# Kernel optimization log

Hardware: AMD Instinct MI355X
Metric: run time of the kernel (lower is better)

The kernel has to match this reference:

```python
import jax, jax.numpy as jnp
import numpy as np

B, S, H, E, V = 256, 512, 512, 128, 30000
RNN_IN = H + E + 1  # weighted context + id embedding + rate


def setup_inputs() -> dict:
    key = jax.random.key(0)
    ks = jax.random.split(key, 16)
    nrm = lambda k, shape, s=0.02: jax.random.normal(k, shape, dtype=jnp.float32) * s
    return {
        "input_id": jax.random.randint(ks[0], (B, 1), 0, V),
        "input_rate": jax.random.uniform(ks[1], (B, 1), dtype=jnp.float32),
        "hidden": nrm(ks[2], (1, B, H), 1.0),
        "encoder_outputs": nrm(ks[3], (S, B, H), 1.0),
        "attn_mask": jax.random.randint(ks[4], (B, S), 0, 2),
        "constraint_vec": (jax.random.uniform(ks[5], (B, V)) > 0.3).astype(jnp.float32),
        "emb_id": nrm(ks[6], (V, E)),
        "attn_w": nrm(ks[7], (2 * H, H)),
        "attn_b": jnp.zeros((H,), jnp.float32),
        "v_w": nrm(ks[8], (H,)),
        "w_ih": nrm(ks[9], (3 * H, RNN_IN)),
        "w_hh": nrm(ks[10], (3 * H, H)),
        "b_ih": jnp.zeros((3 * H,), jnp.float32),
        "b_hh": jnp.zeros((3 * H,), jnp.float32),
        "fc_id_w": nrm(ks[11], (H, V)),
        "fc_id_b": jnp.zeros((V,), jnp.float32),
        "tandem_w": nrm(ks[12], (E + H, H)),
        "tandem_b": jnp.zeros((H,), jnp.float32),
        "rate_w": nrm(ks[13], (H, 1)),
        "rate_b": jnp.zeros((1,), jnp.float32),
    }


def reference(input_id, input_rate, hidden, encoder_outputs, attn_mask,
              constraint_vec, emb_id, attn_w, attn_b, v_w,
              w_ih, w_hh, b_ih, b_hh, fc_id_w, fc_id_b,
              tandem_w, tandem_b, rate_w, rate_b):
    hd = hidden.shape[-1]
    h0 = hidden[0]                                # [B, H]
    embedded = emb_id[input_id[:, 0]]             # [B, E] (dropout p=0 -> identity)

    # --- additive attention (concat-linear split to avoid [B,S,2H] concat) ---
    enc = jnp.transpose(encoder_outputs, (1, 0, 2))         # [B, S, H]
    hid_part = h0 @ attn_w[:hd]                             # [B, H]
    enc_part = jnp.einsum('bsh,hk->bsk', enc, attn_w[hd:])  # [B, S, H]
    energy = jnp.tanh(hid_part[:, None, :] + enc_part + attn_b)
    scores = jnp.einsum('bsh,h->bs', energy, v_w)           # [B, S]
    scores = jnp.where(attn_mask == 0, jnp.float32(-1e10), scores)
    a = jax.nn.softmax(scores, axis=1)
    weighted = jnp.einsum('bs,bsh->bh', a, enc)             # [B, H]

    # --- GRU cell (torch gate order: r, z, n) ---
    x = jnp.concatenate([weighted, embedded, input_rate], axis=1)  # [B, H+E+1]
    gi = x @ w_ih.T + b_ih
    gh = h0 @ w_hh.T + b_hh
    gi_r, gi_z, gi_n = jnp.split(gi, 3, axis=1)
    gh_r, gh_z, gh_n = jnp.split(gh, 3, axis=1)
    r = jax.nn.sigmoid(gi_r + gh_r)
    z = jax.nn.sigmoid(gi_z + gh_z)
    n = jnp.tanh(gi_n + r * gh_n)
    h1 = (1.0 - z) * n + z * h0                   # [B, H]

    # --- masked log-softmax over id vocabulary ---
    logits = h1 @ fc_id_w + fc_id_b               # [B, V]
    maxes = jnp.max(logits, axis=1, keepdims=True)
    x_exp = jnp.exp(logits - maxes) * constraint_vec
    pred = jnp.clip(x_exp / jnp.sum(x_exp, axis=1, keepdims=True), 1e-6, 1.0)
    prediction_id = jnp.log(pred)

    # --- tandem rate head ---
    max_id = jnp.argmax(prediction_id, axis=1)
    id_emb = emb_id[max_id]                       # [B, E]
    rate_in = jax.nn.relu(jnp.concatenate([id_emb, h1], axis=1) @ tandem_w + tandem_b)
    prediction_rate = jax.nn.sigmoid(rate_in @ rate_w + rate_b)  # [B, 1]

    return prediction_id, prediction_rate, h1[None]  # hidden [1, B, H]
```

## Files before the change

### kernel.cpp

```cpp
#include <hip/hip_runtime.h>
#include <hip/hip_bf16.h>

#define B_ 256
#define S_ 512
#define H_ 512
#define E_ 128
#define V_ 30000
#define RNNIN_ 641

using bf16x8 = __attribute__((ext_vector_type(8))) short;
using f32x4  = __attribute__((ext_vector_type(4))) float;

__device__ __forceinline__ short f2bf(float f) {
  unsigned int u = __float_as_uint(f);
  u += 0x7fffu + ((u >> 16) & 1u);
  return (short)(u >> 16);
}

__device__ __forceinline__ float fast_tanh(float x) {
  x = fminf(10.f, fmaxf(-10.f, x));
  float t = __expf(2.f * x);
  return (t - 1.f) / (t + 1.f);
}

__device__ __forceinline__ float sigmoidf(float x) {
  return 1.f / (1.f + __expf(-x));
}

__device__ void gemm_nn_dev(float (*As)[65], float (*Bs)[65],
    const float* __restrict__ A, const float* __restrict__ Bm,
    const float* __restrict__ bias, float* __restrict__ C,
    int M, int N, int K, int m0, int n0)
{
  const int tid = threadIdx.x;
  const int tx = tid & 15, ty = tid >> 4;
  float acc[4][4] = {};
  for (int k0 = 0; k0 < K; k0 += 16) {
    __syncthreads();
    #pragma unroll
    for (int i = 0; i < 4; i++) {
      int e = tid + i * 256;
      int m = e >> 4, k = e & 15;
      float v = 0.f;
      if (m0 + m < M && k0 + k < K) v = A[(size_t)(m0 + m) * K + k0 + k];
      As[k][m] = v;
    }
    #pragma unroll
    for (int i = 0; i < 4; i++) {
      int e = tid + i * 256;
      int k = e >> 6, n = e & 63;
      float v = 0.f;
      if (n0 + n < N && k0 + k < K) v = Bm[(size_t)(k0 + k) * N + n0 + n];
      Bs[k][n] = v;
    }
    __syncthreads();
    #pragma unroll
    for (int k = 0; k < 16; k++) {
      float a[4], b[4];
      #pragma unroll
      for (int i = 0; i < 4; i++) a[i] = As[k][ty * 4 + i];
      #pragma unroll
      for (int j = 0; j < 4; j++) b[j] = Bs[k][tx * 4 + j];
      #pragma unroll
      for (int i = 0; i < 4; i++)
        #pragma unroll
        for (int j = 0; j < 4; j++) acc[i][j] += a[i] * b[j];
    }
  }
  #pragma unroll
  for (int i = 0; i < 4; i++) {
    int m = m0 + ty * 4 + i;
    if (m >= M) continue;
    #pragma unroll
    for (int j = 0; j < 4; j++) {
      int n = n0 + tx * 4 + j;
      if (n >= N) continue;
      C[(size_t)m * N + n] = acc[i][j] + bias[n];
    }
  }
}

__device__ void gemm_bt_dev(float (*As)[65], float (*Bs)[65],
    const float* __restrict__ A, const float* __restrict__ Bm,
    const float* __restrict__ bias, float* __restrict__ C,
    int M, int N, int K)
{
  const int m0 = blockIdx.x * 64, n0 = blockIdx.y * 64;
  const int tid = threadIdx.x;
  const int tx = tid & 15, ty = tid >> 4;
  float acc[4][4] = {};
  for (int k0 = 0; k0 < K; k0 += 16) {
    __syncthreads();
    #pragma unroll
    for (int i = 0; i < 4; i++) {
      int e = tid + i * 256;
      int m = e >> 4, k = e & 15;
      float v = 0.f;
      if (m0 + m < M && k0 + k < K) v = A[(size_t)(m0 + m) * K + k0 + k];
      As[k][m] = v;
    }
    #pragma unroll
    for (int i = 0; i < 4; i++) {
      int e = tid + i * 256;
      int n = e >> 4, k = e & 15;
      float v = 0.f;
      if (n0 + n < N && k0 + k < K) v = Bm[(size_t)(n0 + n) * K + k0 + k];
      Bs[k][n] = v;
    }
    __syncthreads();
    #pragma unroll
    for (int k = 0; k < 16; k++) {
      float a[4], b[4];
      #pragma unroll
      for (int i = 0; i < 4; i++) a[i] = As[k][ty * 4 + i];
      #pragma unroll
      for (int j = 0; j < 4; j++) b[j] = Bs[k][tx * 4 + j];
      #pragma unroll
      for (int i = 0; i < 4; i++)
        #pragma unroll
        for (int j = 0; j < 4; j++) acc[i][j] += a[i] * b[j];
    }
  }
  #pragma unroll
  for (int i = 0; i < 4; i++) {
    int m = m0 + ty * 4 + i;
    if (m >= M) continue;
    #pragma unroll
    for (int j = 0; j < 4; j++) {
      int n = n0 + tx * 4 + j;
      if (n >= N) continue;
      C[(size_t)m * N + n] = acc[i][j] + bias[n];
    }
  }
}

__global__ __launch_bounds__(256) void prep_fused(
    const float* __restrict__ attn_w, unsigned short* __restrict__ Btf,
    const float* __restrict__ hidden, const float* __restrict__ attn_b,
    float* __restrict__ hid_pb)
{
  __shared__ float As[16][65];
  __shared__ float Bs[16][65];
  int bid = blockIdx.x;
  if (bid < 1024) {
    int i = bid * 256 + threadIdx.x;
    int k = i >> 9, n = i & 511;
    float v = attn_w[(size_t)H_ * H_ + i];
    int idx = ((((k >> 5) * 32 + (n >> 4)) * 4 + ((k >> 3) & 3)) * 16 + (n & 15)) * 8 + (k & 7);
    Btf[idx] = (unsigned short)f2bf(v);
  } else {
    int bb = bid - 1024;
    gemm_nn_dev(As, Bs, hidden, attn_w, attn_b, hid_pb, B_, H_, H_,
                (bb & 3) * 64, (bb >> 2) * 64);
  }
}

__global__ __launch_bounds__(256) void attn_gemm_score(
    const float* __restrict__ A, const unsigned short* __restrict__ Btf,
    const float* __restrict__ hid_pb, const float* __restrict__ v_w,
    float* __restrict__ scores)
{
  __shared__ short As[2 * 4096];

  const int bid  = blockIdx.x;
  const int tile = (bid & 7) * 512 + (bid >> 3);
  const int mblk = tile >> 1, nblk = tile & 1;
  const int m0 = mblk * 64, n0 = nblk * 256;

  const int tid  = threadIdx.x;
  const int lane = tid & 63;
  const int wv   = tid >> 6;
  const int quad = lane >> 4, l15 = lane & 15;

  const int arow = tid >> 2, aseg = tid & 3;
  const float* aptr = A + (size_t)(m0 + arow) * H_ + aseg * 16;
  const int ac = aseg >> 1, aq0 = (aseg & 1) * 2;
  short* aw0 = &As[((ac * 4 + (arow >> 4)) * 64 + aq0 * 16 + (arow & 15)) * 8];

  const int nf0 = nblk * 16 + wv * 4;

  f32x4 acc[4][4];
  #pragma unroll
  for (int i = 0; i < 4; i++)
    #pragma unroll
    for (int j = 0; j < 4; j++) acc[i][j] = f32x4{0.f, 0.f, 0.f, 0.f};

  float4 rA[4];
  #pragma unroll
  for (int i = 0; i < 4; i++) rA[i] = *(const float4*)(aptr + i * 4);

  #pragma unroll
  for (int kt = 0; kt < 8; kt++) {
    bf16x8 b[2][4];
    #pragma unroll
    for (int kc = 0; kc < 2; kc++)
      #pragma unroll
      for (int tj = 0; tj < 4; tj++)
        b[kc][tj] = *(const bf16x8*)(Btf + (((kt * 2 + kc) * 32 + nf0 + tj) << 9) + lane * 8);

    {
      bf16x8 f0, f1;
      f0[0] = f2bf(rA[0].x); f0[1] = f2bf(rA[0].y); f0[2] = f2bf(rA[0].z); f0[3] = f2bf(rA[0].w);
      f0[4] = f2bf(rA[1].x); f0[5] = f2bf(rA[1].y); f0[6] = f2bf(rA[1].z); f0[7] = f2bf(rA[1].w);
      f1[0] = f2bf(rA[2].x); f1[1] = f2bf(rA[2].y); f1[2] = f2bf(rA[2].z); f1[3] = f2bf(rA[2].w);
      f1[4] = f2bf(rA[3].x); f1[5] = f2bf(rA[3].y); f1[6] = f2bf(rA[3].z); f1[7] = f2bf(rA[3].w);
      *(bf16x8*)(aw0 + (kt & 1) * 4096)       = f0;
      *(bf16x8*)(aw0 + (kt & 1) * 4096 + 128) = f1;
    }

    if (kt < 7) {
      const float* an = aptr + (kt + 1) * 64;
      #pragma unroll
      for (int i = 0; i < 4; i++) rA[i] = *(const float4*)(an + i * 4);
    }

    asm volatile("s_waitcnt lgkmcnt(0)" ::: "memory");
    __builtin_amdgcn_s_barrier();
    __builtin_amdgcn_sched_barrier(0);

    const short* ab = &As[(kt & 1) * 4096];
    #pragma unroll
    for (int kc = 0; kc < 2; kc++) {
      bf16x8 a[4];
      #pragma unroll
      for (int mi = 0; mi < 4; mi++)
        a[mi] = *(const bf16x8*)&ab[((kc * 4 + mi) * 64 + lane) * 8];
      #pragma unroll
      for (int mi = 0; mi < 4; mi++)
        #pragma unroll
        for (int tj = 0; tj < 4; tj++)
          acc[mi][tj] = __builtin_amdgcn_mfma_f32_16x16x32_bf16(a[mi], b[kc][tj], acc[mi][tj], 0, 0, 0);
    }
  }

  __syncthreads();
  float* part = (float*)As;
  #pragma unroll
  for (int ti = 0; ti < 4; ti++) {
    #pragma unroll
    for (int r = 0; r < 4; r++) {
      int m = m0 + ti * 16 + quad * 4 + r;
      int b = m & (B_ - 1);
      float sum = 0.f;
      #pragma unroll
      for (int tj = 0; tj < 4; tj++) {
        int n = n0 + wv * 64 + tj * 16 + l15;
        float v = acc[ti][tj][r] + hid_pb[b * H_ + n];
        sum += fast_tanh(v) * v_w[n];
      }
      sum += __shfl_xor(sum, 1);
      sum += __shfl_xor(sum, 2);
      sum += __shfl_xor(sum, 4);
      sum += __shfl_xor(sum, 8);
      if (l15 == 0) part[(ti * 16 + quad * 4 + r) * 4 + wv] = sum;
    }
  }
  __syncthreads();
  if (tid < 64) {
    float s4 = part[tid * 4 + 0] + part[tid * 4 + 1] + part[tid * 4 + 2] + part[tid * 4 + 3];
    int m = m0 + tid;
    atomicAdd(scores + (m & (B_ - 1)) * S_ + (m >> 8), s4);
  }
}

__global__ __launch_bounds__(256) void gemm_gru(
    const float* __restrict__ xb, const float* __restrict__ w_ih,
    const float* __restrict__ b_ih, float* __restrict__ gi,
    const float* __restrict__ hid, const float* __restrict__ w_hh,
    const float* __restrict__ b_hh, float* __restrict__ gh)
{
  __shared__ float As[16][65];
  __shared__ float Bs[16][65];
  if (blockIdx.z == 0) gemm_bt_dev(As, Bs, xb, w_ih, b_ih, gi, B_, 1536, RNNIN_);
  else                 gemm_bt_dev(As, Bs, hid, w_hh, b_hh, gh, B_, 1536, H_);
}

__global__ __launch_bounds__(256, 4) void logits_gemm(
    const unsigned short* __restrict__ Ab, const float* __restrict__ Bw,
    const float* __restrict__ bias, float* __restrict__ C)
{
  __shared__ short As[2 * 16 * 64 * 8];
  __shared__ short Bs[2 * 4 * 64 * 8];
  const int n0 = blockIdx.x * 64;
  const int tid = threadIdx.x;
  const int lane = tid & 63;
  const int wv = tid >> 6;
  const int quad = lane >> 4, l15 = lane & 15;

  f32x4 acc[4][4];
  #pragma unroll
  for (int i = 0; i < 4; i++)
    #pragma unroll
    for (int j = 0; j < 4; j++) acc[i][j] = f32x4{0.f, 0.f, 0.f, 0.f};

  const int nB  = tid & 63;
  const int kg  = tid >> 6;
  const int cB  = kg >> 1;
  const int q0  = (kg & 1) * 2;
  const int tjB = nB >> 4;
  const bool nOK = (n0 + nB) < V_;

  for (int kt = 0; kt < 8; kt++) {
    const int kb = kt * 64;
    __syncthreads();
    #pragma unroll
    for (int p = 0; p < 8; p++) {
      int m = p * 32 + (tid >> 3), f = tid & 7;
      int c = f >> 2, q = f & 3;
      bf16x8 v = *(const bf16x8*)(Ab + (size_t)m * H_ + kb + c * 32 + q * 8);
      int mt = m >> 4, ld = q * 16 + (m & 15);
      *(bf16x8*)&As[((c * 16 + mt) * 64 + ld) * 8] = v;
    }
    {
      float col[16];
      const float* src = Bw + (size_t)(kb + kg * 16) * V_ + n0 + nB;
      #pragma unroll
      for (int i = 0; i < 16; i++) col[i] = nOK ? src[(size_t)i * V_] : 0.f;
      bf16x8 f0, f1;
      #pragma unroll
      for (int i = 0; i < 8; i++) { f0[i] = f2bf(col[i]); f1[i] = f2bf(col[8 + i]); }
      int ld0 = q0 * 16 + (nB & 15);
      *(bf16x8*)&Bs[((cB * 4 + tjB) * 64 + ld0) * 8] = f0;
      *(bf16x8*)&Bs[((cB * 4 + tjB) * 64 + ld0 + 16) * 8] = f1;
    }
    __syncthreads();
    #pragma unroll
    for (int c = 0; c < 2; c++) {
      bf16x8 a[4], b[4];
      #pragma unroll
      for (int ti = 0; ti < 4; ti++)
        a[ti] = *(const bf16x8*)&As[((c * 16 + wv * 4 + ti) * 64 + lane) * 8];
      #pragma unroll
      for (int tj = 0; tj < 4; tj++)
        b[tj] = *(const bf16x8*)&Bs[((c * 4 + tj) * 64 + lane) * 8];
      #pragma unroll
      for (int ti = 0; ti < 4; ti++)
        #pragma unroll
        for (int tj = 0; tj < 4; tj++)
          acc[ti][tj] = __builtin_amdgcn_mfma_f32_16x16x32_bf16(a[ti], b[tj], acc[ti][tj], 0, 0, 0);
    }
  }
  #pragma unroll
  for (int ti = 0; ti < 4; ti++)
    #pragma unroll
    for (int r = 0; r < 4; r++) {
      int m = wv * 64 + ti * 16 + quad * 4 + r;
      #pragma unroll
      for (int tj = 0; tj < 4; tj++) {
        int n = n0 + tj * 16 + l15;
        if (n < V_) C[(size_t)m * V_ + n] = acc[ti][tj][r] + bias[n];
      }
    }
}

__global__ __launch_bounds__(256) void attn_softmax(
    const float* __restrict__ scores, const int* __restrict__ mask, float* __restrict__ aw)
{
  int b = blockIdx.x, tid = threadIdx.x;
  __shared__ float red[256];
  float v0 = scores[b * S_ + tid];
  float v1 = scores[b * S_ + tid + 256];
  if (mask[b * S_ + tid] == 0) v0 = -1e10f;
  if (mask[b * S_ + tid + 256] == 0) v1 = -1e10f;
  red[tid] = fmaxf(v0, v1);
  __syncthreads();
  for (int off = 128; off; off >>= 1) { if (tid < off) red[tid] = fmaxf(red[tid], red[tid + off]); __syncthreads(); }
  float mx = red[0];
  __syncthreads();
  float e0 = __expf(v0 - mx), e1 = __expf(v1 - mx);
  red[tid] = e0 + e1;
  __syncthreads();
  for (int off = 128; off; off >>= 1) { if (tid < off) red[tid] += red[tid + off]; __syncthreads(); }
  float inv = 1.f / red[0];
  aw[b * S_ + tid] = e0 * inv;
  aw[b * S_ + tid + 256] = e1 * inv;
}

__global__ __launch_bounds__(512) void attn_weighted_part(
    const float* __restrict__ aw, const float* __restrict__ enc, float* __restrict__ wpart)
{
  int b = blockIdx.x, c = blockIdx.y, h = threadIdx.x;
  __shared__ float a_s[64];
  if (h < 64) a_s[h] = aw[b * S_ + c * 64 + h];
  __syncthreads();
  const float* ep = enc + ((size_t)(c * 64) * B_ + b) * H_ + h;
  float acc = 0.f;
  #pragma unroll 8
  for (int s = 0; s < 64; s++)
    acc += a_s[s] * ep[(size_t)s * B_ * H_];
  wpart[((size_t)c * B_ + b) * H_ + h] = acc;
}

__global__ void build_x(const float* __restrict__ wpart, const int* __restrict__ ids,
                        const float* __restrict__ emb, const float* __restrict__ rate,
                        float* __restrict__ x)
{
  int i = blockIdx.x * 256 + threadIdx.x;
  if (i >= B_ * RNNIN_) return;
  int b = i / RNNIN_, j = i % RNNIN_;
  float v;
  if (j < H_) {
    size_t o = (size_t)b * H_ + j;
    const size_t st = (size_t)B_ * H_;
    v = 0.f;
    #pragma unroll
    for (int c = 0; c < 8; c++) v += wpart[o + c * st];
  }
  else if (j < H_ + E_) v = emb[(size_t)ids[b] * E_ + (j - H_)];
  else v = rate[b];
  x[i] = v;
}

__global__ void gru_gates(const float* __restrict__ gi, const float* __restrict__ gh,
                          const float* __restrict__ h0, float* __restrict__ h1,
                          unsigned short* __restrict__ h1b, float* __restrict__ h1_out)
{
  int i = blockIdx.x * 256 + threadIdx.x;
  int b = i >> 9, j = i & (H_ - 1);
  const float* gib = gi + (size_t)b * 1536;
  const float* ghb = gh + (size_t)b * 1536;
  float r = sigmoidf(gib[j] + ghb[j]);
  float z = sigmoidf(gib[512 + j] + ghb[512 + j]);
  float n = fast_tanh(gib[1024 + j] + r * ghb[1024 + j]);
  float h = (1.f - z) * n + z * h0[i];
  h1[i] = h;
  h1b[i] = (unsigned short)f2bf(h);
  h1_out[i] = h;
}

__global__ __launch_bounds__(1024) void softmax_fused(
    float* __restrict__ lp, const float* __restrict__ cv, int* __restrict__ maxid)
{
  int b = blockIdx.x, tid = threadIdx.x;
  int wid = tid >> 6, lane = tid & 63;
  float* row = lp + (size_t)b * V_;
  const float* cvr = cv + (size_t)b * V_;
  __shared__ float redf[16];
  __shared__ float rede[16];
  __shared__ int   redi[16];

  float mx = -INFINITY;
  for (int v = tid; v < V_; v += 1024) mx = fmaxf(mx, row[v]);
  #pragma unroll
  for (int o = 1; o < 64; o <<= 1) mx = fmaxf(mx, __shfl_xor(mx, o));
  if (lane == 0) redf[wid] = mx;
  __syncthreads();
  if (tid == 0) {
    float m = redf[0];
    for (int i = 1; i < 16; i++) m = fmaxf(m, redf[i]);
    redf[0] = m;
  }
  __syncthreads();
  float M = redf[0];
  __syncthreads();

  float s = 0.f, best = -1.f;
  int bi = 0;
  for (int v = tid; v < V_; v += 1024) {
    float e = __expf(row[v] - M) * cvr[v];
    row[v] = e;
    s += e;
    if (e > best) { best = e; bi = v; }
  }
  #pragma unroll
  for (int o = 1; o < 64; o <<= 1) {
    s += __shfl_xor(s, o);
    float ob = __shfl_xor(best, o);
    int oi = __shfl_xor(bi, o);
    if (ob > best || (ob == best && oi < bi)) { best = ob; bi = oi; }
  }
  if (lane == 0) { redf[wid] = s; rede[wid] = best; redi[wid] = bi; }
  __syncthreads();
  if (tid == 0) {
    float ss = 0.f, bb = rede[0];
    int ii = redi[0];
    for (int i = 0; i < 16; i++) {
      ss += redf[i];
      if (rede[i] > bb || (rede[i] == bb && redi[i] < ii)) { bb = rede[i]; ii = redi[i]; }
    }
    redf[0] = ss;
    maxid[b] = ii;
  }
  __syncthreads();
  float inv = 1.f / redf[0];
  for (int v = tid; v < V_; v += 1024) {
    float p = row[v] * inv;
    p = fminf(fmaxf(p, 1e-6f), 1.f);
    row[v] = __logf(p);
  }
}

__global__ __launch_bounds__(256) void tandem_gemm(
    const int* __restrict__ maxid, const float* __restrict__ emb,
    const float* __restrict__ h1, const float* __restrict__ tan_w,
    const float* __restrict__ tan_b, float* __restrict__ rate_in)
{
  __shared__ float As[16][65];
  __shared__ float Bs[16][65];
  const int m0 = blockIdx.x * 64, n0 = blockIdx.y * 64;
  const int tid = threadIdx.x;
  const int tx = tid & 15, ty = tid >> 4;
  float acc[4][4] = {};
  for (int k0 = 0; k0 < 640; k0 += 16) {
    __syncthreads();
    #pragma unroll
    for (int i = 0; i < 4; i++) {
      int e = tid + i * 256;
      int m = e >> 4, kk = e & 15;
      int mm = m0 + m, k = k0 + kk;
      float v = (k < E_) ? emb[(size_t)maxid[mm] * E_ + k]
                         : h1[(size_t)mm * H_ + (k - E_)];
      As[kk][m] = v;
    }
    #pragma unroll
    for (int i = 0; i < 4; i++) {
      int e = tid + i * 256;
      int k = e >> 6, n = e & 63;
      Bs[k][n] = tan_w[(size_t)(k0 + k) * H_ + n0 + n];
    }
    __syncthreads();
    #pragma unroll
    for (int k = 0; k < 16; k++) {
      float a[4], b[4];
      #pragma unroll
      for (int i = 0; i < 4; i++) a[i] = As[k][ty * 4 + i];
      #pragma unroll
      for (int j = 0; j < 4; j++) b[j] = Bs[k][tx * 4 + j];
      #pragma unroll
      for (int i = 0; i < 4; i++)
        #pragma unroll
        for (int j = 0; j < 4; j++) acc[i][j] += a[i] * b[j];
    }
  }
  #pragma unroll
  for (int i = 0; i < 4; i++) {
    int m = m0 + ty * 4 + i;
    #pragma unroll
    for (int j = 0; j < 4; j++) {
      int n = n0 + tx * 4 + j;
      rate_in[(size_t)m * H_ + n] = fmaxf(acc[i][j] + tan_b[n], 0.f);
    }
  }
}

__global__ __launch_bounds__(64) void rate_head(const float* __restrict__ rate_in,
                                                const float* __restrict__ rate_w,
                                                const float* __restrict__ rate_b,
                                                float* __restrict__ out)
{
  int b = blockIdx.x, t = threadIdx.x;
  float s = 0.f;
  #pragma unroll
  for (int i = 0; i < 8; i++) s += rate_in[b * H_ + t + 64 * i] * rate_w[t + 64 * i];
  #pragma unroll
  for (int m = 32; m; m >>= 1) s += __shfl_xor(s, m);
  if (t == 0) out[b] = sigmoidf(s + rate_b[0]);
}

extern "C" void kernel_launch(void* const* d_in, const int* in_sizes, int n_in,
                              void* d_out, int out_size, void* d_ws, size_t ws_size,
                              hipStream_t stream)
{
  const int*   input_id   = (const int*)  d_in[0];
  const float* input_rate = (const float*)d_in[1];
  const float* hidden     = (const float*)d_in[2];
  const float* enc        = (const float*)d_in[3];
  const int*   attn_mask  = (const int*)  d_in[4];
  const float* cv         = (const float*)d_in[5];
  const float* emb        = (const float*)d_in[6];
  const float* attn_w     = (const float*)d_in[7];
  const float* attn_b     = (const float*)d_in[8];
  const float* v_w        = (const float*)d_in[9];
  const float* w_ih       = (const float*)d_in[10];
  const float* w_hh       = (const float*)d_in[11];
  const float* b_ih       = (const float*)d_in[12];
  const float* b_hh       = (const float*)d_in[13];
  const float* fc_w       = (const float*)d_in[14];
  const float* fc_b       = (const float*)d_in[15];
  const float* tan_w      = (const float*)d_in[16];
  const float* tan_b      = (const float*)d_in[17];
  const float* rate_w     = (const float*)d_in[18];
  const float* rate_b     = (const float*)d_in[19];

  float* out = (float*)d_out;
  float* ws  = (float*)d_ws;
  float* hid_pb   = ws;
  float* scores   = ws + 131072;
  float* aw       = ws + 262144;
  float* xbuf     = ws + 524288;
  float* gi       = ws + 688384;
  float* gh       = ws + 1081600;
  float* h1       = ws + 1474816;
  float* rate_in  = ws + 1605888;
  int*   maxid    = (int*)(ws + 1736960);
  unsigned short* Btf = (unsigned short*)(ws + 1737216);
  unsigned short* h1b = (unsigned short*)(ws + 1868288);
  float* wpart = gi;

  float* out_pred = out;
  float* out_rate = out + (size_t)B_ * V_;
  float* out_h1   = out + (size_t)B_ * V_ + B_;

  hipMemsetAsync(scores, 0, (size_t)B_ * S_ * sizeof(float), stream);

  prep_fused<<<1056, 256, 0, stream>>>(attn_w, Btf, hidden, attn_b, hid_pb);

  attn_gemm_score<<<4096, 256, 0, stream>>>(enc, Btf, hid_pb, v_w, scores);

  attn_softmax<<<B_, 256, 0, stream>>>(scores, attn_mask, aw);
  attn_weighted_part<<<dim3(B_, 8), 512, 0, stream>>>(aw, enc, wpart);
  build_x<<<641, 256, 0, stream>>>(wpart, input_id, emb, input_rate, xbuf);

  gemm_gru<<<dim3(4, 24, 2), 256, 0, stream>>>(xbuf, w_ih, b_ih, gi, hidden, w_hh, b_hh, gh);
  gru_gates<<<512, 256, 0, stream>>>(gi, gh, hidden, h1, h1b, out_h1);

  logits_gemm<<<469, 256, 0, stream>>>(h1b, fc_w, fc_b, out_pred);
  softmax_fused<<<B_, 1024, 0, stream>>>(out_pred, cv, maxid);

  tandem_gemm<<<dim3(4, 8), 256, 0, stream>>>(maxid, emb, h1, tan_w, tan_b, rate_in);
  rate_head<<<B_, 64, 0, stream>>>(rate_in, rate_w, rate_b, out_rate);
}
```

Measured before the change: 1.004 ms.

## Restructure attention score GEMM as persistent 512-thread blocks with LDS-resident weights

The attention score kernel now uses 1024 blocks of 512 threads. Each block loads a 128-column quarter of the bf16 attention weight matrix once into 128KB of LDS via global_load_lds and then loops over four 128-row tiles of encoder outputs. This removes the repeated per-tile global reads of B fragments. The encoder rows are prefetched in registers across k-steps and across tiles. In exchange, the large LDS footprint limits occupancy to one block per CU, and the per-k-step barriers with a small MFMA count per step may expose latency.

Measured after the change: 1.084 ms. 7.9% more time.

```diff
diff --git a/kernel.cpp b/kernel.cpp
--- a/kernel.cpp
+++ b/kernel.cpp
@@ -25,6 +25,12 @@
 
 __device__ __forceinline__ float sigmoidf(float x) {
   return 1.f / (1.f + __expf(-x));
+}
+
+__device__ __forceinline__ void gload_lds16(const void* g, void* l) {
+  __builtin_amdgcn_global_load_lds(
+      (const __attribute__((address_space(1))) void*)g,
+      (__attribute__((address_space(3))) void*)l, 16, 0, 0);
 }
 
 __device__ void gemm_nn_dev(float (*As)[65], float (*Bs)[65],
@@ -155,112 +161,149 @@
   }
 }
 
-__global__ __launch_bounds__(256) void attn_gemm_score(
+__global__ __launch_bounds__(512) void attn_gemm_score(
     const float* __restrict__ A, const unsigned short* __restrict__ Btf,
     const float* __restrict__ hid_pb, const float* __restrict__ v_w,
     float* __restrict__ scores)
 {
-  __shared__ short As[2 * 4096];
-
-  const int bid  = blockIdx.x;
-  const int tile = (bid & 7) * 512 + (bid >> 3);
-  const int mblk = tile >> 1, nblk = tile & 1;
-  const int m0 = mblk * 64, n0 = nblk * 256;
+  __shared__ short Bs[65536];
+  __shared__ short Abuf[8192];
+
+  const int bid = blockIdx.x;
+  const int w   = bid >> 8;
+  const int i8  = bid & 255;
+  const int q   = (i8 >> 3) & 3;
+  const int mg  = w * 64 + (i8 >> 5) * 8 + (i8 & 7);
+  const int nq0 = q * 128;
 
   const int tid  = threadIdx.x;
   const int lane = tid & 63;
   const int wv   = tid >> 6;
+  const int wr   = wv >> 2;
+  const int wc   = wv & 3;
   const int quad = lane >> 4, l15 = lane & 15;
 
-  const int arow = tid >> 2, aseg = tid & 3;
-  const float* aptr = A + (size_t)(m0 + arow) * H_ + aseg * 16;
-  const int ac = aseg >> 1, aq0 = (aseg & 1) * 2;
-  short* aw0 = &As[((ac * 4 + (arow >> 4)) * 64 + aq0 * 16 + (arow & 15)) * 8];
-
-  const int nf0 = nblk * 16 + wv * 4;
-
-  f32x4 acc[4][4];
-  #pragma unroll
-  for (int i = 0; i < 4; i++)
-    #pragma unroll
-    for (int j = 0; j < 4; j++) acc[i][j] = f32x4{0.f, 0.f, 0.f, 0.f};
-
-  float4 rA[4];
-  #pragma unroll
-  for (int i = 0; i < 4; i++) rA[i] = *(const float4*)(aptr + i * 4);
-
-  #pragma unroll
-  for (int kt = 0; kt < 8; kt++) {
-    bf16x8 b[2][4];
-    #pragma unroll
-    for (int kc = 0; kc < 2; kc++)
-      #pragma unroll
-      for (int tj = 0; tj < 4; tj++)
-        b[kc][tj] = *(const bf16x8*)(Btf + (((kt * 2 + kc) * 32 + nf0 + tj) << 9) + lane * 8);
-
-    {
-      bf16x8 f0, f1;
-      f0[0] = f2bf(rA[0].x); f0[1] = f2bf(rA[0].y); f0[2] = f2bf(rA[0].z); f0[3] = f2bf(rA[0].w);
-      f0[4] = f2bf(rA[1].x); f0[5] = f2bf(rA[1].y); f0[6] = f2bf(rA[1].z); f0[7] = f2bf(rA[1].w);
-      f1[0] = f2bf(rA[2].x); f1[1] = f2bf(rA[2].y); f1[2] = f2bf(rA[2].z); f1[3] = f2bf(rA[2].w);
-      f1[4] = f2bf(rA[3].x); f1[5] = f2bf(rA[3].y); f1[6] = f2bf(rA[3].z); f1[7] = f2bf(rA[3].w);
-      *(bf16x8*)(aw0 + (kt & 1) * 4096)       = f0;
-      *(bf16x8*)(aw0 + (kt & 1) * 4096 + 128) = f1;
-    }
-
-    if (kt < 7) {
-      const float* an = aptr + (kt + 1) * 64;
-      #pragma unroll
-      for (int i = 0; i < 4; i++) rA[i] = *(const float4*)(an + i * 4);
-    }
-
+  #pragma unroll
+  for (int i = 0; i < 16; i++) {
+    int frag = wv * 16 + i;
+    const unsigned short* g = Btf
+        + ((size_t)((frag >> 3) * 32 + q * 8 + (frag & 7)) << 9) + lane * 8;
+    gload_lds16((const void*)g, (void*)(Bs + (size_t)frag * 512));
+  }
+
+  const int rt = tid >> 2, qs = tid & 3;
+  const float* tb = A + ((size_t)mg * 512 + rt) * H_ + qs * 8;
+  short* awp = Abuf + (((rt >> 4) * 64) + qs * 16 + (rt & 15)) * 8;
+
+  const float vw0 = v_w[nq0 + wc * 32 + l15];
+  const float vw1 = v_w[nq0 + wc * 32 + 16 + l15];
+
+  float4 s0a = *(const float4*)(tb);
+  float4 s0b = *(const float4*)(tb + 4);
+  float4 s1a = *(const float4*)(tb + 32);
+  float4 s1b = *(const float4*)(tb + 36);
+  float4 s2a = *(const float4*)(tb + 64);
+  float4 s2b = *(const float4*)(tb + 68);
+  float4 s3a = *(const float4*)(tb + 96);
+  float4 s3b = *(const float4*)(tb + 100);
+
+  asm volatile("s_waitcnt vmcnt(0)" ::: "memory");
+  __builtin_amdgcn_s_barrier();
+
+  f32x4 acc[4][2];
+  #pragma unroll
+  for (int mi = 0; mi < 4; mi++) {
+    acc[mi][0] = f32x4{0.f, 0.f, 0.f, 0.f};
+    acc[mi][1] = f32x4{0.f, 0.f, 0.f, 0.f};
+  }
+
+#define KT_STEP(kt, SA, SB)                                                   \
+  do {                                                                        \
+    { bf16x8 f;                                                               \
+      f[0] = f2bf(SA.x); f[1] = f2bf(SA.y); f[2] = f2bf(SA.z); f[3] = f2bf(SA.w); \
+      f[4] = f2bf(SB.x); f[5] = f2bf(SB.y); f[6] = f2bf(SB.z); f[7] = f2bf(SB.w); \
+      *(bf16x8*)(awp + ((kt) & 1) * 4096) = f; }                              \
+    if ((kt) < 12) {                                                          \
+      SA = *(const float4*)(tba + ((kt) + 4) * 32);                           \
+      SB = *(const float4*)(tba + ((kt) + 4) * 32 + 4);                       \
+    } else if (t < 3) {                                                       \
+      SA = *(const float4*)(tba + 65536 + ((kt) - 12) * 32);                  \
+      SB = *(const float4*)(tba + 65536 + ((kt) - 12) * 32 + 4);              \
+    }                                                                         \
+    asm volatile("s_waitcnt lgkmcnt(0)" ::: "memory");                        \
+    __builtin_amdgcn_s_barrier();                                             \
+    __builtin_amdgcn_sched_barrier(0);                                        \
+    { const short* ap = Abuf + ((kt) & 1) * 4096 + wr * 2048 + lane * 8;      \
+      bf16x8 a0 = *(const bf16x8*)(ap);                                       \
+      bf16x8 a1 = *(const bf16x8*)(ap + 512);                                 \
+      bf16x8 a2 = *(const bf16x8*)(ap + 1024);                                \
+      bf16x8 a3 = *(const bf16x8*)(ap + 1536);                                \
+      const short* bp = Bs + ((kt) * 8 + wc * 2) * 512 + lane * 8;            \
+      bf16x8 b0 = *(const bf16x8*)(bp);                                       \
+      bf16x8 b1 = *(const bf16x8*)(bp + 512);                                 \
+      acc[0][0] = __builtin_amdgcn_mfma_f32_16x16x32_bf16(a0, b0, acc[0][0], 0, 0, 0); \
+      acc[0][1] = __builtin_amdgcn_mfma_f32_16x16x32_bf16(a0, b1, acc[0][1], 0, 0, 0); \
+      acc[1][0] = __builtin_amdgcn_mfma_f32_16x16x32_bf16(a1, b0, acc[1][0], 0, 0, 0); \
+      acc[1][1] = __builtin_amdgcn_mfma_f32_16x16x32_bf16(a1, b1, acc[1][1], 0, 0, 0); \
+      acc[2][0] = __builtin_amdgcn_mfma_f32_16x16x32_bf16(a2, b0, acc[2][0], 0, 0, 0); \
+      acc[2][1] = __builtin_amdgcn_mfma_f32_16x16x32_bf16(a2, b1, acc[2][1], 0, 0, 0); \
+      acc[3][0] = __builtin_amdgcn_mfma_f32_16x16x32_bf16(a3, b0, acc[3][0], 0, 0, 0); \
+      acc[3][1] = __builtin_amdgcn_mfma_f32_16x16x32_bf16(a3, b1, acc[3][1], 0, 0, 0); \
+    }                                                                         \
+  } while (0)
+
+  for (int t = 0; t < 4; t++) {
+    const float* tba = tb + (size_t)t * 65536;
+    const int m0 = mg * 512 + t * 128;
+
+    KT_STEP(0,  s0a, s0b);  KT_STEP(1,  s1a, s1b);
+    KT_STEP(2,  s2a, s2b);  KT_STEP(3,  s3a, s3b);
+    KT_STEP(4,  s0a, s0b);  KT_STEP(5,  s1a, s1b);
+    KT_STEP(6,  s2a, s2b);  KT_STEP(7,  s3a, s3b);
+    KT_STEP(8,  s0a, s0b);  KT_STEP(9,  s1a, s1b);
+    KT_STEP(10, s2a, s2b);  KT_STEP(11, s3a, s3b);
+    KT_STEP(12, s0a, s0b);  KT_STEP(13, s1a, s1b);
+    KT_STEP(14, s2a, s2b);  KT_STEP(15, s3a, s3b);
+
+    float* part = (float*)Abuf;
+    #pragma unroll
+    for (int mi = 0; mi < 4; mi++) {
+      #pragma unroll
+      for (int r = 0; r < 4; r++) {
+        int row16 = mi * 16 + quad * 4 + r;
+        int m = m0 + wr * 64 + row16;
+        int b = m & (B_ - 1);
+        int n0l = nq0 + wc * 32 + l15;
+        float e0 = acc[mi][0][r] + hid_pb[b * H_ + n0l];
+        float e1 = acc[mi][1][r] + hid_pb[b * H_ + n0l + 16];
+        float sum = fast_tanh(e0) * vw0 + fast_tanh(e1) * vw1;
+        sum += __shfl_xor(sum, 1);
+        sum += __shfl_xor(sum, 2);
+        sum += __shfl_xor(sum, 4);
+        sum += __shfl_xor(sum, 8);
+        if (l15 == 0) part[(wr * 64 + row16) * 4 + wc] = sum;
+      }
+    }
     asm volatile("s_waitcnt lgkmcnt(0)" ::: "memory");
     __builtin_amdgcn_s_barrier();
     __builtin_amdgcn_sched_barrier(0);
-
-    const short* ab = &As[(kt & 1) * 4096];
-    #pragma unroll
-    for (int kc = 0; kc < 2; kc++) {
-      bf16x8 a[4];
-      #pragma unroll
-      for (int mi = 0; mi < 4; mi++)
-        a[mi] = *(const bf16x8*)&ab[((kc * 4 + mi) * 64 + lane) * 8];
-      #pragma unroll
-      for (int mi = 0; mi < 4; mi++)
-        #pragma unroll
-        for (int tj = 0; tj < 4; tj++)
-          acc[mi][tj] = __builtin_amdgcn_mfma_f32_16x16x32_bf16(a[mi], b[kc][tj], acc[mi][tj], 0, 0, 0);
-    }
-  }
-
-  __syncthreads();
-  float* part = (float*)As;
-  #pragma unroll
-  for (int ti = 0; ti < 4; ti++) {
-    #pragma unroll
-    for (int r = 0; r < 4; r++) {
-      int m = m0 + ti * 16 + quad * 4 + r;
-      int b = m & (B_ - 1);
-      float sum = 0.f;
-      #pragma unroll
-      for (int tj = 0; tj < 4; tj++) {
-        int n = n0 + wv * 64 + tj * 16 + l15;
-        float v = acc[ti][tj][r] + hid_pb[b * H_ + n];
-        sum += fast_tanh(v) * v_w[n];
-      }
-      sum += __shfl_xor(sum, 1);
-      sum += __shfl_xor(sum, 2);
-      sum += __shfl_xor(sum, 4);
-      sum += __shfl_xor(sum, 8);
-      if (l15 == 0) part[(ti * 16 + quad * 4 + r) * 4 + wv] = sum;
-    }
-  }
-  __syncthreads();
-  if (tid < 64) {
-    float s4 = part[tid * 4 + 0] + part[tid * 4 + 1] + part[tid * 4 + 2] + part[tid * 4 + 3];
-    int m = m0 + tid;
-    atomicAdd(scores + (m & (B_ - 1)) * S_ + (m >> 8), s4);
-  }
+    if (tid < 128) {
+      float s4 = part[tid * 4 + 0] + part[tid * 4 + 1]
+               + part[tid * 4 + 2] + part[tid * 4 + 3];
+      int m = m0 + tid;
+      atomicAdd(scores + (m & (B_ - 1)) * S_ + (m >> 8), s4);
+    }
+    asm volatile("s_waitcnt lgkmcnt(0)" ::: "memory");
+    __builtin_amdgcn_s_barrier();
+    __builtin_amdgcn_sched_barrier(0);
+
+    #pragma unroll
+    for (int mi = 0; mi < 4; mi++) {
+      acc[mi][0] = f32x4{0.f, 0.f, 0.f, 0.f};
+      acc[mi][1] = f32x4{0.f, 0.f, 0.f, 0.f};
+    }
+  }
+#undef KT_STEP
 }
 
 __global__ __launch_bounds__(256) void gemm_gru(
@@ -306,9 +349,9 @@
     #pragma unroll
     for (int p = 0; p < 8; p++) {
       int m = p * 32 + (tid >> 3), f = tid & 7;
-      int c = f >> 2, q = f & 3;
-      bf16x8 v = *(const bf16x8*)(Ab + (size_t)m * H_ + kb + c * 32 + q * 8);
-      int mt = m >> 4, ld = q * 16 + (m & 15);
+      int c = f >> 2, qq = f & 3;
+      bf16x8 v = *(const bf16x8*)(Ab + (size_t)m * H_ + kb + c * 32 + qq * 8);
+      int mt = m >> 4, ld = qq * 16 + (m & 15);
       *(bf16x8*)&As[((c * 16 + mt) * 64 + ld) * 8] = v;
     }
     {
@@ -605,7 +648,7 @@
 
   prep_fused<<<1056, 256, 0, stream>>>(attn_w, Btf, hidden, attn_b, hid_pb);
 
-  attn_gemm_score<<<4096, 256, 0, stream>>>(enc, Btf, hid_pb, v_w, scores);
+  attn_gemm_score<<<1024, 512, 0, stream>>>(enc, Btf, hid_pb, v_w, scores);
 
   attn_softmax<<<B_, 256, 0, stream>>>(scores, attn_mask, aw);
   attn_weighted_part<<<dim3(B_, 8), 512, 0, stream>>>(aw, enc, wpart);
```

## Widen attention score blocks to full N, drop atomics and memset, use packed bf16 converts

Applied to the files above, without the earlier changes.

The attention GEMM+score kernel now uses 512-thread blocks that each cover all 512 output columns for 64 rows. Each row's score is then reduced fully in-block and written directly, which removes the atomicAdd accumulation and the memset of the scores buffer. The encoder A tile is converted and staged once per row block instead of twice, with a two-stage register prefetch. Float-to-bf16 conversion switches to the hardware packed convert instruction in both GEMMs, and tanh loses its clamp and uses a single division. Larger blocks may reduce occupancy, and the unclamped tanh relies on exp overflow saturating correctly.

New measurement: 981.8 us. 1.02x faster.

```diff
diff --git a/kernel.cpp b/kernel.cpp
--- a/kernel.cpp
+++ b/kernel.cpp
@@ -17,10 +17,15 @@
   return (short)(u >> 16);
 }
 
+__device__ __forceinline__ unsigned cvtpk(float a, float b) {
+  unsigned r;
+  asm("v_cvt_pk_bf16_f32 %0, %1, %2" : "=v"(r) : "v"(a), "v"(b));
+  return r;
+}
+
 __device__ __forceinline__ float fast_tanh(float x) {
-  x = fminf(10.f, fmaxf(-10.f, x));
   float t = __expf(2.f * x);
-  return (t - 1.f) / (t + 1.f);
+  return 1.f - 2.f / (t + 1.f);
 }
 
 __device__ __forceinline__ float sigmoidf(float x) {
@@ -155,29 +160,23 @@
   }
 }
 
-__global__ __launch_bounds__(256) void attn_gemm_score(
+__global__ __launch_bounds__(512) void attn_gemm_score(
     const float* __restrict__ A, const unsigned short* __restrict__ Btf,
     const float* __restrict__ hid_pb, const float* __restrict__ v_w,
     float* __restrict__ scores)
 {
-  __shared__ short As[2 * 4096];
-
-  const int bid  = blockIdx.x;
-  const int tile = (bid & 7) * 512 + (bid >> 3);
-  const int mblk = tile >> 1, nblk = tile & 1;
-  const int m0 = mblk * 64, n0 = nblk * 256;
-
+  __shared__ short Abuf[2 * 4096];
+
+  const int m0 = blockIdx.x * 64;
   const int tid  = threadIdx.x;
   const int lane = tid & 63;
   const int wv   = tid >> 6;
   const int quad = lane >> 4, l15 = lane & 15;
 
-  const int arow = tid >> 2, aseg = tid & 3;
-  const float* aptr = A + (size_t)(m0 + arow) * H_ + aseg * 16;
-  const int ac = aseg >> 1, aq0 = (aseg & 1) * 2;
-  short* aw0 = &As[((ac * 4 + (arow >> 4)) * 64 + aq0 * 16 + (arow & 15)) * 8];
-
-  const int nf0 = nblk * 16 + wv * 4;
+  const int rt = tid >> 3, qs = tid & 7;
+  const float* aptr = A + ((size_t)(m0 + rt)) * H_ + qs * 8;
+  const int kc = qs >> 2, qq = qs & 3;
+  short* awp = Abuf + ((kc * 4 + (rt >> 4)) * 64 + qq * 16 + (rt & 15)) * 8;
 
   f32x4 acc[4][4];
   #pragma unroll
@@ -185,81 +184,93 @@
     #pragma unroll
     for (int j = 0; j < 4; j++) acc[i][j] = f32x4{0.f, 0.f, 0.f, 0.f};
 
-  float4 rA[4];
-  #pragma unroll
-  for (int i = 0; i < 4; i++) rA[i] = *(const float4*)(aptr + i * 4);
-
-  #pragma unroll
-  for (int kt = 0; kt < 8; kt++) {
-    bf16x8 b[2][4];
-    #pragma unroll
-    for (int kc = 0; kc < 2; kc++)
-      #pragma unroll
-      for (int tj = 0; tj < 4; tj++)
-        b[kc][tj] = *(const bf16x8*)(Btf + (((kt * 2 + kc) * 32 + nf0 + tj) << 9) + lane * 8);
-
-    {
-      bf16x8 f0, f1;
-      f0[0] = f2bf(rA[0].x); f0[1] = f2bf(rA[0].y); f0[2] = f2bf(rA[0].z); f0[3] = f2bf(rA[0].w);
-      f0[4] = f2bf(rA[1].x); f0[5] = f2bf(rA[1].y); f0[6] = f2bf(rA[1].z); f0[7] = f2bf(rA[1].w);
-      f1[0] = f2bf(rA[2].x); f1[1] = f2bf(rA[2].y); f1[2] = f2bf(rA[2].z); f1[3] = f2bf(rA[2].w);
-      f1[4] = f2bf(rA[3].x); f1[5] = f2bf(rA[3].y); f1[6] = f2bf(rA[3].z); f1[7] = f2bf(rA[3].w);
-      *(bf16x8*)(aw0 + (kt & 1) * 4096)       = f0;
-      *(bf16x8*)(aw0 + (kt & 1) * 4096 + 128) = f1;
-    }
-
-    if (kt < 7) {
-      const float* an = aptr + (kt + 1) * 64;
-      #pragma unroll
-      for (int i = 0; i < 4; i++) rA[i] = *(const float4*)(an + i * 4);
-    }
-
-    asm volatile("s_waitcnt lgkmcnt(0)" ::: "memory");
-    __builtin_amdgcn_s_barrier();
-    __builtin_amdgcn_sched_barrier(0);
-
-    const short* ab = &As[(kt & 1) * 4096];
-    #pragma unroll
-    for (int kc = 0; kc < 2; kc++) {
-      bf16x8 a[4];
-      #pragma unroll
-      for (int mi = 0; mi < 4; mi++)
-        a[mi] = *(const bf16x8*)&ab[((kc * 4 + mi) * 64 + lane) * 8];
-      #pragma unroll
-      for (int mi = 0; mi < 4; mi++)
-        #pragma unroll
-        for (int tj = 0; tj < 4; tj++)
-          acc[mi][tj] = __builtin_amdgcn_mfma_f32_16x16x32_bf16(a[mi], b[kc][tj], acc[mi][tj], 0, 0, 0);
-    }
-  }
-
-  __syncthreads();
-  float* part = (float*)As;
-  #pragma unroll
-  for (int ti = 0; ti < 4; ti++) {
+  float4 p0a = *(const float4*)(aptr);
+  float4 p0b = *(const float4*)(aptr + 4);
+  float4 p1a = *(const float4*)(aptr + 64);
+  float4 p1b = *(const float4*)(aptr + 68);
+
+#define KT_STEP(kt, PA, PB)                                                   \
+  do {                                                                        \
+           \
+    bf16x8 b[2][4];                                                           \
+    _Pragma("unroll")                                                         \
+    for (int kcc = 0; kcc < 2; kcc++)                                         \
+      _Pragma("unroll")                                                       \
+      for (int tj = 0; tj < 4; tj++)                                          \
+        b[kcc][tj] = *(const bf16x8*)(Btf                                     \
+            + ((((kt) * 2 + kcc) * 32 + wv * 4 + tj) << 9) + lane * 8);       \
+                  \
+    { uint4 pk;                                                               \
+      pk.x = cvtpk(PA.x, PA.y); pk.y = cvtpk(PA.z, PA.w);                     \
+      pk.z = cvtpk(PB.x, PB.y); pk.w = cvtpk(PB.z, PB.w);                     \
+      *(uint4*)(awp + ((kt) & 1) * 4096) = pk; }                              \
+                    \
+    if ((kt) < 6) {                                                           \
+      PA = *(const float4*)(aptr + ((kt) + 2) * 64);                          \
+      PB = *(const float4*)(aptr + ((kt) + 2) * 64 + 4);                      \
+    }                                                                         \
+    asm volatile("s_waitcnt lgkmcnt(0)" ::: "memory");                        \
+    __builtin_amdgcn_s_barrier();                                             \
+    __builtin_amdgcn_sched_barrier(0);                                        \
+    { const short* ab = Abuf + ((kt) & 1) * 4096;                             \
+      _Pragma("unroll")                                                       \
+      for (int kcc = 0; kcc < 2; kcc++) {                                     \
+        bf16x8 a[4];                                                          \
+        _Pragma("unroll")                                                     \
+        for (int mi = 0; mi < 4; mi++)                                        \
+          a[mi] = *(const bf16x8*)&ab[((kcc * 4 + mi) * 64 + lane) * 8];      \
+        _Pragma("unroll")                                                     \
+        for (int mi = 0; mi < 4; mi++)                                        \
+          _Pragma("unroll")                                                   \
+          for (int tj = 0; tj < 4; tj++)                                      \
+            acc[mi][tj] = __builtin_amdgcn_mfma_f32_16x16x32_bf16(            \
+                a[mi], b[kcc][tj], acc[mi][tj], 0, 0, 0);                     \
+      }                                                                       \
+    }                                                                         \
+  } while (0)
+
+  KT_STEP(0, p0a, p0b);  KT_STEP(1, p1a, p1b);
+  KT_STEP(2, p0a, p0b);  KT_STEP(3, p1a, p1b);
+  KT_STEP(4, p0a, p0b);  KT_STEP(5, p1a, p1b);
+  KT_STEP(6, p0a, p0b);  KT_STEP(7, p1a, p1b);
+#undef KT_STEP
+
+  const float vw0 = v_w[wv * 64 + l15];
+  const float vw1 = v_w[wv * 64 + 16 + l15];
+  const float vw2 = v_w[wv * 64 + 32 + l15];
+  const float vw3 = v_w[wv * 64 + 48 + l15];
+
+  float* part = (float*)Abuf;
+  #pragma unroll
+  for (int mi = 0; mi < 4; mi++) {
     #pragma unroll
     for (int r = 0; r < 4; r++) {
-      int m = m0 + ti * 16 + quad * 4 + r;
+      int row16 = mi * 16 + quad * 4 + r;
+      int m = m0 + row16;
       int b = m & (B_ - 1);
-      float sum = 0.f;
-      #pragma unroll
-      for (int tj = 0; tj < 4; tj++) {
-        int n = n0 + wv * 64 + tj * 16 + l15;
-        float v = acc[ti][tj][r] + hid_pb[b * H_ + n];
-        sum += fast_tanh(v) * v_w[n];
-      }
+      const float* hp = hid_pb + (size_t)b * H_ + wv * 64 + l15;
+      float e0 = acc[mi][0][r] + hp[0];
+      float e1 = acc[mi][1][r] + hp[16];
+      float e2 = acc[mi][2][r] + hp[32];
+      float e3 = acc[mi][3][r] + hp[48];
+      float sum = fast_tanh(e0) * vw0 + fast_tanh(e1) * vw1
+                + fast_tanh(e2) * vw2 + fast_tanh(e3) * vw3;
       sum += __shfl_xor(sum, 1);
       sum += __shfl_xor(sum, 2);
       sum += __shfl_xor(sum, 4);
       sum += __shfl_xor(sum, 8);
-      if (l15 == 0) part[(ti * 16 + quad * 4 + r) * 4 + wv] = sum;
-    }
-  }
-  __syncthreads();
+      if (l15 == 0) part[row16 * 8 + wv] = sum;
+    }
+  }
+  asm volatile("s_waitcnt lgkmcnt(0)" ::: "memory");
+  __builtin_amdgcn_s_barrier();
+  __builtin_amdgcn_sched_barrier(0);
   if (tid < 64) {
-    float s4 = part[tid * 4 + 0] + part[tid * 4 + 1] + part[tid * 4 + 2] + part[tid * 4 + 3];
+    float s8 = 0.f;
+    #pragma unroll
+    for (int w = 0; w < 8; w++) s8 += part[tid * 8 + w];
     int m = m0 + tid;
-    atomicAdd(scores + (m & (B_ - 1)) * S_ + (m >> 8), s4);
+    scores[(m & (B_ - 1)) * S_ + (m >> 8)] = s8;
   }
 }
 
@@ -306,9 +317,9 @@
     #pragma unroll
     for (int p = 0; p < 8; p++) {
       int m = p * 32 + (tid >> 3), f = tid & 7;
-      int c = f >> 2, q = f & 3;
-      bf16x8 v = *(const bf16x8*)(Ab + (size_t)m * H_ + kb + c * 32 + q * 8);
-      int mt = m >> 4, ld = q * 16 + (m & 15);
+      int c = f >> 2, qq = f & 3;
+      bf16x8 v = *(const bf16x8*)(Ab + (size_t)m * H_ + kb + c * 32 + qq * 8);
+      int mt = m >> 4, ld = qq * 16 + (m & 15);
       *(bf16x8*)&As[((c * 16 + mt) * 64 + ld) * 8] = v;
     }
     {
@@ -316,12 +327,14 @@
       const float* src = Bw + (size_t)(kb + kg * 16) * V_ + n0 + nB;
       #pragma unroll
       for (int i = 0; i < 16; i++) col[i] = nOK ? src[(size_t)i * V_] : 0.f;
-      bf16x8 f0, f1;
-      #pragma unroll
-      for (int i = 0; i < 8; i++) { f0[i] = f2bf(col[i]); f1[i] = f2bf(col[8 + i]); }
+      uint4 f0, f1;
+      f0.x = cvtpk(col[0],  col[1]);  f0.y = cvtpk(col[2],  col[3]);
+      f0.z = cvtpk(col[4],  col[5]);  f0.w = cvtpk(col[6],  col[7]);
+      f1.x = cvtpk(col[8],  col[9]);  f1.y = cvtpk(col[10], col[11]);
+      f1.z = cvtpk(col[12], col[13]); f1.w = cvtpk(col[14], col[15]);
       int ld0 = q0 * 16 + (nB & 15);
-      *(bf16x8*)&Bs[((cB * 4 + tjB) * 64 + ld0) * 8] = f0;
-      *(bf16x8*)&Bs[((cB * 4 + tjB) * 64 + ld0 + 16) * 8] = f1;
+      *(uint4*)&Bs[((cB * 4 + tjB) * 64 + ld0) * 8] = f0;
+      *(uint4*)&Bs[((cB * 4 + tjB) * 64 + ld0 + 16) * 8] = f1;
     }
     __syncthreads();
     #pragma unroll
@@ -601,11 +614,9 @@
   float* out_rate = out + (size_t)B_ * V_;
   float* out_h1   = out + (size_t)B_ * V_ + B_;
 
-  hipMemsetAsync(scores, 0, (size_t)B_ * S_ * sizeof(float), stream);
-
   prep_fused<<<1056, 256, 0, stream>>>(attn_w, Btf, hidden, attn_b, hid_pb);
 
-  attn_gemm_score<<<4096, 256, 0, stream>>>(enc, Btf, hid_pb, v_w, scores);
+  attn_gemm_score<<<2048, 512, 0, stream>>>(enc, Btf, hid_pb, v_w, scores);
 
   attn_softmax<<<B_, 256, 0, stream>>>(scores, attn_mask, aw);
   attn_weighted_part<<<dim3(B_, 8), 512, 0, stream>>>(aw, enc, wpart);
```
